# Optimization experiments

Hardware: AMD Instinct MI355X
Metric: run time of the kernel (lower is better)

Reference implementation:

```python
import jax, jax.numpy as jnp
import numpy as np

SLIDING_WINDOW = 2048
NUM_SINK = 4


def make_mask(q_len, k_len, dtype=jnp.float32):
    # positions of queries in the key axis
    q_pos = jnp.arange(k_len - q_len, k_len)[:, None]  # [Q,1]
    k_pos = jnp.arange(k_len)[None, :]                 # [1,K]
    causal = k_pos <= q_pos
    in_window = k_pos >= (q_pos - SLIDING_WINDOW + 1)
    is_sink = k_pos < NUM_SINK
    allowed = causal & (in_window | is_sink)
    return jnp.where(allowed, jnp.zeros((), dtype), jnp.full((), -jnp.inf, dtype))


def setup_inputs() -> dict:
    key = jax.random.key(0)
    k1, k2, k3 = jax.random.split(key, 3)
    B, H, L, D = 2, 16, 4096, 128
    q = jax.random.normal(k1, (B, H, L, D), dtype=jnp.float32)
    k = jax.random.normal(k2, (B, H, L, D), dtype=jnp.float32)
    v = jax.random.normal(k3, (B, H, L, D), dtype=jnp.float32)
    return {"q": q, "k": k, "v": v}


def reference(q, k, v):
    B, H, L, D = q.shape
    mask = make_mask(L, k.shape[2], q.dtype)  # [L, L] additive
    scale = 1.0 / jnp.sqrt(jnp.asarray(D, q.dtype))
    scores = jnp.einsum('bhqd,bhkd->bhqk', q, k) * scale + mask
    probs = jax.nn.softmax(scores, axis=-1)
    return jnp.einsum('bhqk,bhkd->bhqd', probs, v)
```

## Files before the change

kernel.cpp:

```cpp
#include <hip/hip_runtime.h>

constexpr int Ld = 4096;
constexpr int Dd = 128;
constexpr int BQ = 128;
constexpr int BK = 64;
constexpr int WSZ = 2048;
constexpr int NSINK = 4;
constexpr float QSCALE = 0.08838834764831845f * 1.4426950408889634f;

typedef short bf16x8 __attribute__((ext_vector_type(8)));
typedef float f32x4 __attribute__((ext_vector_type(4)));

#if defined(__has_builtin)
#if __has_builtin(__builtin_amdgcn_exp2f)
#define EXP2(x) __builtin_amdgcn_exp2f(x)
#endif
#endif
#ifndef EXP2
#define EXP2(x) exp2f(x)
#endif

__device__ __forceinline__ unsigned pkbf(float hi, float lo) {
    unsigned r;
    asm("v_cvt_pk_bf16_f32 %0, %1, %2" : "=v"(r) : "v"(lo), "v"(hi));
    return r;
}

__device__ __forceinline__ int rd_off(int row, int d) {
    return row * 128 + ((((d >> 3) ^ row) & 15) << 3) + (d & 7);
}
__device__ __forceinline__ int vt_off(int drow, int key) {
    return drow * 64 + ((((key >> 3) ^ drow) & 7) << 3) + (key & 7);
}
__device__ __forceinline__ int p_off(int row, int key) {
    return row * 64 + ((((key >> 2) ^ ((row & 7) << 1)) & 15) << 2) + (key & 3);
}

__global__ __launch_bounds__(256, 2)
void swa_fwd(const float* __restrict__ Qg, const float* __restrict__ Kg,
             const float* __restrict__ Vg, float* __restrict__ Og) {
    __shared__ __align__(16) unsigned short smem[24576];
    unsigned short* Ks  = smem;
    unsigned short* Vts = smem + 8192;
    unsigned short* Ps  = smem + 16384;
    unsigned short* Qst = smem;

    const int tid  = threadIdx.x;
    const int w    = tid >> 6;
    const int lane = tid & 63;
    const int ml   = lane & 15;
    const int quad = lane >> 4;

    const int qtile = (int)(gridDim.x - 1u - blockIdx.x);
    const int q0 = qtile * BQ;
    const int bh = blockIdx.y;

    const size_t baseQ  = ((size_t)bh * Ld + q0) * Dd;
    const size_t baseKV = (size_t)bh * Ld * Dd;

    #pragma unroll
    for (int i = 0; i < 16; ++i) {
        int idx = tid + i * 256;
        int row = idx >> 5;
        int d0  = (idx & 31) << 2;
        float4 v = *(const float4*)(Qg + baseQ + (size_t)row * Dd + d0);
        *(uint2*)&Qst[rd_off(row, d0)] =
            make_uint2(pkbf(v.y * QSCALE, v.x * QSCALE),
                       pkbf(v.w * QSCALE, v.z * QSCALE));
    }
    __syncthreads();

    bf16x8 qf[2][4];
    #pragma unroll
    for (int g = 0; g < 2; ++g)
        #pragma unroll
        for (int k0 = 0; k0 < 4; ++k0)
            qf[g][k0] = *(const bf16x8*)&Qst[rd_off(w * 32 + g * 16 + ml,
                                                    k0 * 32 + quad * 8)];

    float l_i[2] = {0.f, 0.f};
    f32x4 o_acc[2][8];
    #pragma unroll
    for (int g = 0; g < 2; ++g)
        #pragma unroll
        for (int dt = 0; dt < 8; ++dt)
            o_acc[g][dt] = (f32x4){0.f, 0.f, 0.f, 0.f};

    const int kmin = (q0 - (WSZ - 1)) > 0 ? (q0 - (WSZ - 1)) : 0;
    const int kb_first = (kmin / BK) * BK;
    const bool sink_extra = (kb_first > 0);
    const int nch = (q0 + BQ - kb_first) / BK + (sink_extra ? 1 : 0);

    const int qrow0 = q0 + w * 32 + ml;
    unsigned short* Pw = Ps + w * 2048;

    float4 kreg[8];
    float  vreg[32];
    const int kr0 = tid >> 5;
    const int kd0 = (tid & 31) << 2;
    const int vd  = tid & 127;
    const int vkh = tid >> 7;

    auto kvload = [&](int kb) {
        const float* kp = Kg + baseKV + (size_t)(kb + kr0) * Dd + kd0;
        #pragma unroll
        for (int i = 0; i < 8; ++i)
            kreg[i] = *(const float4*)(kp + (size_t)i * 8 * Dd);
        const float* vp = Vg + baseKV + (size_t)(kb + vkh * 32) * Dd + vd;
        #pragma unroll
        for (int j = 0; j < 32; ++j)
            vreg[j] = vp[(size_t)j * Dd];
    };
    auto kb_of = [&](int ci) {
        return sink_extra ? (ci == 0 ? 0 : kb_first + (ci - 1) * BK)
                          : kb_first + ci * BK;
    };

    kvload(kb_of(0));

    for (int ci = 0; ci < nch; ++ci) {
        const int kb = kb_of(ci);

        __syncthreads();

        #pragma unroll
        for (int i = 0; i < 8; ++i)
            *(uint2*)&Ks[rd_off(kr0 + i * 8, kd0)] =
                make_uint2(pkbf(kreg[i].y, kreg[i].x),
                           pkbf(kreg[i].w, kreg[i].z));
        #pragma unroll
        for (int m2 = 0; m2 < 4; ++m2) {
            *(uint4*)&Vts[vt_off(vd, vkh * 32 + m2 * 8)] =
                make_uint4(pkbf(vreg[m2 * 8 + 1], vreg[m2 * 8 + 0]),
                           pkbf(vreg[m2 * 8 + 3], vreg[m2 * 8 + 2]),
                           pkbf(vreg[m2 * 8 + 5], vreg[m2 * 8 + 4]),
                           pkbf(vreg[m2 * 8 + 7], vreg[m2 * 8 + 6]));
        }
        __syncthreads();

        if (ci + 1 < nch) kvload(kb_of(ci + 1));

        f32x4 s[2][4];
        #pragma unroll
        for (int g = 0; g < 2; ++g)
            #pragma unroll
            for (int t = 0; t < 4; ++t)
                s[g][t] = (f32x4){0.f, 0.f, 0.f, 0.f};
        #pragma unroll
        for (int k0 = 0; k0 < 4; ++k0) {
            bf16x8 ka[4];
            #pragma unroll
            for (int t = 0; t < 4; ++t)
                ka[t] = *(const bf16x8*)&Ks[rd_off(t * 16 + ml, k0 * 32 + quad * 8)];
            #pragma unroll
            for (int t = 0; t < 4; ++t) {
                s[0][t] = __builtin_amdgcn_mfma_f32_16x16x32_bf16(ka[t], qf[0][k0], s[0][t], 0, 0, 0);
                s[1][t] = __builtin_amdgcn_mfma_f32_16x16x32_bf16(ka[t], qf[1][k0], s[1][t], 0, 0, 0);
            }
        }

        const bool full = (kb + (BK - 1) <= q0) && (kb + (WSZ - BQ) >= q0 - 1);

        #pragma unroll
        for (int g = 0; g < 2; ++g) {
            const int q = qrow0 + g * 16;
            if (!full) {
                #pragma unroll
                for (int t = 0; t < 4; ++t)
                    #pragma unroll
                    for (int r = 0; r < 4; ++r) {
                        int k = kb + t * 16 + quad * 4 + r;
                        bool ok = (k <= q) && ((k + (WSZ - 1) >= q) || (k < NSINK));
                        s[g][t][r] = ok ? s[g][t][r] : -3e38f;
                    }
            }
            float rs = 0.f;
            #pragma unroll
            for (int t = 0; t < 4; ++t)
                #pragma unroll
                for (int r = 0; r < 4; ++r) {
                    float p = EXP2(s[g][t][r]);
                    s[g][t][r] = p;
                    rs += p;
                }
            l_i[g] += rs;

            unsigned short* Pg = Pw + g * 1024;
            #pragma unroll
            for (int t = 0; t < 4; ++t)
                *(uint2*)&Pg[p_off(ml, t * 16 + quad * 4)] =
                    make_uint2(pkbf(s[g][t][1], s[g][t][0]),
                               pkbf(s[g][t][3], s[g][t][2]));
        }

        #pragma unroll
        for (int k0 = 0; k0 < 2; ++k0) {
            bf16x8 pb0 = *(const bf16x8*)&Pw[p_off(ml, k0 * 32 + quad * 8)];
            bf16x8 pb1 = *(const bf16x8*)&Pw[1024 + p_off(ml, k0 * 32 + quad * 8)];
            #pragma unroll
            for (int dt = 0; dt < 8; ++dt) {
                bf16x8 va = *(const bf16x8*)&Vts[vt_off(dt * 16 + ml, k0 * 32 + quad * 8)];
                o_acc[0][dt] = __builtin_amdgcn_mfma_f32_16x16x32_bf16(va, pb0, o_acc[0][dt], 0, 0, 0);
                o_acc[1][dt] = __builtin_amdgcn_mfma_f32_16x16x32_bf16(va, pb1, o_acc[1][dt], 0, 0, 0);
            }
        }
    }

    #pragma unroll
    for (int g = 0; g < 2; ++g) {
        float lt = l_i[g];
        lt += __shfl_xor(lt, 16);
        lt += __shfl_xor(lt, 32);
        const float inv = 1.f / lt;
        float* op = Og + ((size_t)bh * Ld + (qrow0 + g * 16)) * Dd;
        #pragma unroll
        for (int dt = 0; dt < 8; ++dt) {
            float4 o;
            o.x = o_acc[g][dt][0] * inv;
            o.y = o_acc[g][dt][1] * inv;
            o.z = o_acc[g][dt][2] * inv;
            o.w = o_acc[g][dt][3] * inv;
            *(float4*)(op + dt * 16 + quad * 4) = o;
        }
    }
}

extern "C" void kernel_launch(void* const* d_in, const int* in_sizes, int n_in,
                              void* d_out, int out_size, void* d_ws, size_t ws_size,
                              hipStream_t stream) {
    const float* q = (const float*)d_in[0];
    const float* k = (const float*)d_in[1];
    const float* v = (const float*)d_in[2];
    float* o = (float*)d_out;
    const int bhn = in_sizes[0] / (Ld * Dd);
    dim3 grid(Ld / BQ, bhn);
    swa_fwd<<<grid, dim3(256, 1, 1), 0, stream>>>(q, k, v, o);
}
```

Measured before the change: 400.6 us.

## Pre-convert K/V to swizzled bf16 and stream tiles via async global-to-LDS loads

Adds a pre-pass kernel that converts K and V to bf16 once, with K in the swizzled row layout and V pre-transposed per 64-key block, and writes both into the workspace. The attention kernel then double-buffers K/V tiles in LDS using global_load_lds direct copies, which removes the per-tile fp32 register staging, repeated conversion, and one barrier per iteration. It also remaps workgroups with an XCD-aware 1D grid and raises wave priority around the MFMA sections. The trade-offs are an extra launch plus a bf16 write and read of K/V, and a larger LDS footprint (80 KB) that may limit occupancy to the two blocks the launch bounds target.

New measurement: 340.0 us. -15.1%, faster.

```diff
diff --git a/kernel.cpp b/kernel.cpp
--- a/kernel.cpp
+++ b/kernel.cpp
@@ -36,13 +36,58 @@
     return row * 64 + ((((key >> 2) ^ ((row & 7) << 1)) & 15) << 2) + (key & 3);
 }
 
+typedef const __attribute__((address_space(1))) unsigned int* gas1_t;
+typedef __attribute__((address_space(3))) unsigned int* las3_t;
+__device__ __forceinline__ void lds16(const void* g, void* l) {
+    __builtin_amdgcn_global_load_lds((gas1_t)g, (las3_t)l, 16, 0, 0);
+}
+
+__global__ __launch_bounds__(256)
+void cvt_kv(const float* __restrict__ Kg, const float* __restrict__ Vg,
+            unsigned short* __restrict__ Kw, unsigned short* __restrict__ Vw) {
+    __shared__ __align__(16) unsigned short vt[8192];
+    const int tid = threadIdx.x;
+    const int kb = blockIdx.x * BK;
+    const int bh = blockIdx.y;
+    const size_t gbase = ((size_t)bh * Ld + kb) * Dd;
+
+    #pragma unroll
+    for (int i = 0; i < 8; ++i) {
+        int id = tid + i * 256;
+        int row = id >> 5;
+        int d0 = (id & 31) << 2;
+        float4 a = *(const float4*)(Kg + gbase + (size_t)row * Dd + d0);
+        *(uint2*)&Kw[gbase + rd_off(row, d0)] =
+            make_uint2(pkbf(a.y, a.x), pkbf(a.w, a.z));
+    }
+
+    const int vd  = tid & 127;
+    const int vkh = tid >> 7;
+    const float* vp = Vg + gbase + (size_t)vkh * 32 * Dd + vd;
+    float vr[32];
+    #pragma unroll
+    for (int j = 0; j < 32; ++j) vr[j] = vp[(size_t)j * Dd];
+    #pragma unroll
+    for (int m2 = 0; m2 < 4; ++m2)
+        *(uint4*)&vt[vt_off(vd, vkh * 32 + m2 * 8)] =
+            make_uint4(pkbf(vr[m2 * 8 + 1], vr[m2 * 8 + 0]),
+                       pkbf(vr[m2 * 8 + 3], vr[m2 * 8 + 2]),
+                       pkbf(vr[m2 * 8 + 5], vr[m2 * 8 + 4]),
+                       pkbf(vr[m2 * 8 + 7], vr[m2 * 8 + 6]));
+    __syncthreads();
+    const size_t vbase = ((size_t)bh * (Ld / BK) + blockIdx.x) * (size_t)(BK * Dd);
+    #pragma unroll
+    for (int i = 0; i < 4; ++i) {
+        int j = tid + i * 256;
+        *(uint4*)&Vw[vbase + (size_t)j * 8] = *(const uint4*)&vt[j * 8];
+    }
+}
+
 __global__ __launch_bounds__(256, 2)
-void swa_fwd(const float* __restrict__ Qg, const float* __restrict__ Kg,
-             const float* __restrict__ Vg, float* __restrict__ Og) {
-    __shared__ __align__(16) unsigned short smem[24576];
-    unsigned short* Ks  = smem;
-    unsigned short* Vts = smem + 8192;
-    unsigned short* Ps  = smem + 16384;
+void swa_fwd2(const float* __restrict__ Qg, const unsigned short* __restrict__ Kw,
+              const unsigned short* __restrict__ Vw, float* __restrict__ Og) {
+    __shared__ __align__(16) unsigned short smem[40960];
+    unsigned short* Ps  = smem + 32768;
     unsigned short* Qst = smem;
 
     const int tid  = threadIdx.x;
@@ -51,12 +96,16 @@
     const int ml   = lane & 15;
     const int quad = lane >> 4;
 
-    const int qtile = (int)(gridDim.x - 1u - blockIdx.x);
+    const unsigned wgr = blockIdx.x;
+    const unsigned nwg = gridDim.x;
+    unsigned wgid = wgr;
+    if ((nwg & 7u) == 0u) wgid = (wgr & 7u) * (nwg >> 3) + (wgr >> 3);
+    const int tpb   = Ld / BQ;
+    const int bh    = (int)(wgid / (unsigned)tpb);
+    const int qtile = tpb - 1 - (int)(wgid % (unsigned)tpb);
     const int q0 = qtile * BQ;
-    const int bh = blockIdx.y;
-
-    const size_t baseQ  = ((size_t)bh * Ld + q0) * Dd;
-    const size_t baseKV = (size_t)bh * Ld * Dd;
+
+    const size_t baseQ = ((size_t)bh * Ld + q0) * Dd;
 
     #pragma unroll
     for (int i = 0; i < 16; ++i) {
@@ -77,6 +126,7 @@
         for (int k0 = 0; k0 < 4; ++k0)
             qf[g][k0] = *(const bf16x8*)&Qst[rd_off(w * 32 + g * 16 + ml,
                                                     k0 * 32 + quad * 8)];
+    __syncthreads();
 
     float l_i[2] = {0.f, 0.f};
     f32x4 o_acc[2][8];
@@ -94,51 +144,35 @@
     const int qrow0 = q0 + w * 32 + ml;
     unsigned short* Pw = Ps + w * 2048;
 
-    float4 kreg[8];
-    float  vreg[32];
-    const int kr0 = tid >> 5;
-    const int kd0 = (tid & 31) << 2;
-    const int vd  = tid & 127;
-    const int vkh = tid >> 7;
-
-    auto kvload = [&](int kb) {
-        const float* kp = Kg + baseKV + (size_t)(kb + kr0) * Dd + kd0;
-        #pragma unroll
-        for (int i = 0; i < 8; ++i)
-            kreg[i] = *(const float4*)(kp + (size_t)i * 8 * Dd);
-        const float* vp = Vg + baseKV + (size_t)(kb + vkh * 32) * Dd + vd;
-        #pragma unroll
-        for (int j = 0; j < 32; ++j)
-            vreg[j] = vp[(size_t)j * Dd];
-    };
     auto kb_of = [&](int ci) {
         return sink_extra ? (ci == 0 ? 0 : kb_first + (ci - 1) * BK)
                           : kb_first + ci * BK;
     };
-
-    kvload(kb_of(0));
+    const size_t kwbase = (size_t)bh * Ld * Dd;
+    const size_t vwbase = (size_t)bh * (Ld / BK) * (size_t)(BK * Dd);
+
+    auto stage = [&](int ci) {
+        const int b = ci & 1;
+        const int kb = kb_of(ci);
+        const unsigned short* kg = Kw + kwbase + (size_t)kb * Dd + tid * 8;
+        unsigned short* kl = smem + b * 8192 + tid * 8;
+        const unsigned short* vg = Vw + vwbase + (size_t)(kb >> 6) * (BK * Dd) + tid * 8;
+        unsigned short* vl = smem + 16384 + b * 8192 + tid * 8;
+        #pragma unroll
+        for (int i = 0; i < 4; ++i) lds16(kg + i * 2048, kl + i * 2048);
+        #pragma unroll
+        for (int i = 0; i < 4; ++i) lds16(vg + i * 2048, vl + i * 2048);
+    };
+
+    stage(0);
 
     for (int ci = 0; ci < nch; ++ci) {
+        __syncthreads();
+        if (ci + 1 < nch) stage(ci + 1);
+
         const int kb = kb_of(ci);
-
-        __syncthreads();
-
-        #pragma unroll
-        for (int i = 0; i < 8; ++i)
-            *(uint2*)&Ks[rd_off(kr0 + i * 8, kd0)] =
-                make_uint2(pkbf(kreg[i].y, kreg[i].x),
-                           pkbf(kreg[i].w, kreg[i].z));
-        #pragma unroll
-        for (int m2 = 0; m2 < 4; ++m2) {
-            *(uint4*)&Vts[vt_off(vd, vkh * 32 + m2 * 8)] =
-                make_uint4(pkbf(vreg[m2 * 8 + 1], vreg[m2 * 8 + 0]),
-                           pkbf(vreg[m2 * 8 + 3], vreg[m2 * 8 + 2]),
-                           pkbf(vreg[m2 * 8 + 5], vreg[m2 * 8 + 4]),
-                           pkbf(vreg[m2 * 8 + 7], vreg[m2 * 8 + 6]));
-        }
-        __syncthreads();
-
-        if (ci + 1 < nch) kvload(kb_of(ci + 1));
+        const unsigned short* Ksb = smem + (ci & 1) * 8192;
+        const unsigned short* Vtb = smem + 16384 + (ci & 1) * 8192;
 
         f32x4 s[2][4];
         #pragma unroll
@@ -146,18 +180,20 @@
             #pragma unroll
             for (int t = 0; t < 4; ++t)
                 s[g][t] = (f32x4){0.f, 0.f, 0.f, 0.f};
+        __builtin_amdgcn_s_setprio(1);
         #pragma unroll
         for (int k0 = 0; k0 < 4; ++k0) {
             bf16x8 ka[4];
             #pragma unroll
             for (int t = 0; t < 4; ++t)
-                ka[t] = *(const bf16x8*)&Ks[rd_off(t * 16 + ml, k0 * 32 + quad * 8)];
+                ka[t] = *(const bf16x8*)&Ksb[rd_off(t * 16 + ml, k0 * 32 + quad * 8)];
             #pragma unroll
             for (int t = 0; t < 4; ++t) {
                 s[0][t] = __builtin_amdgcn_mfma_f32_16x16x32_bf16(ka[t], qf[0][k0], s[0][t], 0, 0, 0);
                 s[1][t] = __builtin_amdgcn_mfma_f32_16x16x32_bf16(ka[t], qf[1][k0], s[1][t], 0, 0, 0);
             }
         }
+        __builtin_amdgcn_s_setprio(0);
 
         const bool full = (kb + (BK - 1) <= q0) && (kb + (WSZ - BQ) >= q0 - 1);
 
@@ -193,6 +229,194 @@
                                pkbf(s[g][t][3], s[g][t][2]));
         }
 
+        __builtin_amdgcn_s_setprio(1);
+        #pragma unroll
+        for (int k0 = 0; k0 < 2; ++k0) {
+            bf16x8 pb0 = *(const bf16x8*)&Pw[p_off(ml, k0 * 32 + quad * 8)];
+            bf16x8 pb1 = *(const bf16x8*)&Pw[1024 + p_off(ml, k0 * 32 + quad * 8)];
+            #pragma unroll
+            for (int dt = 0; dt < 8; ++dt) {
+                bf16x8 va = *(const bf16x8*)&Vtb[vt_off(dt * 16 + ml, k0 * 32 + quad * 8)];
+                o_acc[0][dt] = __builtin_amdgcn_mfma_f32_16x16x32_bf16(va, pb0, o_acc[0][dt], 0, 0, 0);
+                o_acc[1][dt] = __builtin_amdgcn_mfma_f32_16x16x32_bf16(va, pb1, o_acc[1][dt], 0, 0, 0);
+            }
+        }
+        __builtin_amdgcn_s_setprio(0);
+    }
+
+    #pragma unroll
+    for (int g = 0; g < 2; ++g) {
+        float lt = l_i[g];
+        lt += __shfl_xor(lt, 16);
+        lt += __shfl_xor(lt, 32);
+        const float inv = 1.f / lt;
+        float* op = Og + ((size_t)bh * Ld + (qrow0 + g * 16)) * Dd;
+        #pragma unroll
+        for (int dt = 0; dt < 8; ++dt) {
+            float4 o;
+            o.x = o_acc[g][dt][0] * inv;
+            o.y = o_acc[g][dt][1] * inv;
+            o.z = o_acc[g][dt][2] * inv;
+            o.w = o_acc[g][dt][3] * inv;
+            *(float4*)(op + dt * 16 + quad * 4) = o;
+        }
+    }
+}
+
+__global__ __launch_bounds__(256, 2)
+void swa_fwd(const float* __restrict__ Qg, const float* __restrict__ Kg,
+             const float* __restrict__ Vg, float* __restrict__ Og) {
+    __shared__ __align__(16) unsigned short smem[24576];
+    unsigned short* Ks  = smem;
+    unsigned short* Vts = smem + 8192;
+    unsigned short* Ps  = smem + 16384;
+    unsigned short* Qst = smem;
+
+    const int tid  = threadIdx.x;
+    const int w    = tid >> 6;
+    const int lane = tid & 63;
+    const int ml   = lane & 15;
+    const int quad = lane >> 4;
+
+    const int qtile = (int)(gridDim.x - 1u - blockIdx.x);
+    const int q0 = qtile * BQ;
+    const int bh = blockIdx.y;
+
+    const size_t baseQ  = ((size_t)bh * Ld + q0) * Dd;
+    const size_t baseKV = (size_t)bh * Ld * Dd;
+
+    #pragma unroll
+    for (int i = 0; i < 16; ++i) {
+        int idx = tid + i * 256;
+        int row = idx >> 5;
+        int d0  = (idx & 31) << 2;
+        float4 v = *(const float4*)(Qg + baseQ + (size_t)row * Dd + d0);
+        *(uint2*)&Qst[rd_off(row, d0)] =
+            make_uint2(pkbf(v.y * QSCALE, v.x * QSCALE),
+                       pkbf(v.w * QSCALE, v.z * QSCALE));
+    }
+    __syncthreads();
+
+    bf16x8 qf[2][4];
+    #pragma unroll
+    for (int g = 0; g < 2; ++g)
+        #pragma unroll
+        for (int k0 = 0; k0 < 4; ++k0)
+            qf[g][k0] = *(const bf16x8*)&Qst[rd_off(w * 32 + g * 16 + ml,
+                                                    k0 * 32 + quad * 8)];
+
+    float l_i[2] = {0.f, 0.f};
+    f32x4 o_acc[2][8];
+    #pragma unroll
+    for (int g = 0; g < 2; ++g)
+        #pragma unroll
+        for (int dt = 0; dt < 8; ++dt)
+            o_acc[g][dt] = (f32x4){0.f, 0.f, 0.f, 0.f};
+
+    const int kmin = (q0 - (WSZ - 1)) > 0 ? (q0 - (WSZ - 1)) : 0;
+    const int kb_first = (kmin / BK) * BK;
+    const bool sink_extra = (kb_first > 0);
+    const int nch = (q0 + BQ - kb_first) / BK + (sink_extra ? 1 : 0);
+
+    const int qrow0 = q0 + w * 32 + ml;
+    unsigned short* Pw = Ps + w * 2048;
+
+    float4 kreg[8];
+    float  vreg[32];
+    const int kr0 = tid >> 5;
+    const int kd0 = (tid & 31) << 2;
+    const int vd  = tid & 127;
+    const int vkh = tid >> 7;
+
+    auto kvload = [&](int kb) {
+        const float* kp = Kg + baseKV + (size_t)(kb + kr0) * Dd + kd0;
+        #pragma unroll
+        for (int i = 0; i < 8; ++i)
+            kreg[i] = *(const float4*)(kp + (size_t)i * 8 * Dd);
+        const float* vp = Vg + baseKV + (size_t)(kb + vkh * 32) * Dd + vd;
+        #pragma unroll
+        for (int j = 0; j < 32; ++j)
+            vreg[j] = vp[(size_t)j * Dd];
+    };
+    auto kb_of = [&](int ci) {
+        return sink_extra ? (ci == 0 ? 0 : kb_first + (ci - 1) * BK)
+                          : kb_first + ci * BK;
+    };
+
+    kvload(kb_of(0));
+
+    for (int ci = 0; ci < nch; ++ci) {
+        const int kb = kb_of(ci);
+        __syncthreads();
+        #pragma unroll
+        for (int i = 0; i < 8; ++i)
+            *(uint2*)&Ks[rd_off(kr0 + i * 8, kd0)] =
+                make_uint2(pkbf(kreg[i].y, kreg[i].x),
+                           pkbf(kreg[i].w, kreg[i].z));
+        #pragma unroll
+        for (int m2 = 0; m2 < 4; ++m2) {
+            *(uint4*)&Vts[vt_off(vd, vkh * 32 + m2 * 8)] =
+                make_uint4(pkbf(vreg[m2 * 8 + 1], vreg[m2 * 8 + 0]),
+                           pkbf(vreg[m2 * 8 + 3], vreg[m2 * 8 + 2]),
+                           pkbf(vreg[m2 * 8 + 5], vreg[m2 * 8 + 4]),
+                           pkbf(vreg[m2 * 8 + 7], vreg[m2 * 8 + 6]));
+        }
+        __syncthreads();
+        if (ci + 1 < nch) kvload(kb_of(ci + 1));
+
+        f32x4 s[2][4];
+        #pragma unroll
+        for (int g = 0; g < 2; ++g)
+            #pragma unroll
+            for (int t = 0; t < 4; ++t)
+                s[g][t] = (f32x4){0.f, 0.f, 0.f, 0.f};
+        #pragma unroll
+        for (int k0 = 0; k0 < 4; ++k0) {
+            bf16x8 ka[4];
+            #pragma unroll
+            for (int t = 0; t < 4; ++t)
+                ka[t] = *(const bf16x8*)&Ks[rd_off(t * 16 + ml, k0 * 32 + quad * 8)];
+            #pragma unroll
+            for (int t = 0; t < 4; ++t) {
+                s[0][t] = __builtin_amdgcn_mfma_f32_16x16x32_bf16(ka[t], qf[0][k0], s[0][t], 0, 0, 0);
+                s[1][t] = __builtin_amdgcn_mfma_f32_16x16x32_bf16(ka[t], qf[1][k0], s[1][t], 0, 0, 0);
+            }
+        }
+
+        const bool full = (kb + (BK - 1) <= q0) && (kb + (WSZ - BQ) >= q0 - 1);
+
+        #pragma unroll
+        for (int g = 0; g < 2; ++g) {
+            const int q = qrow0 + g * 16;
+            if (!full) {
+                #pragma unroll
+                for (int t = 0; t < 4; ++t)
+                    #pragma unroll
+                    for (int r = 0; r < 4; ++r) {
+                        int k = kb + t * 16 + quad * 4 + r;
+                        bool ok = (k <= q) && ((k + (WSZ - 1) >= q) || (k < NSINK));
+                        s[g][t][r] = ok ? s[g][t][r] : -3e38f;
+                    }
+            }
+            float rs = 0.f;
+            #pragma unroll
+            for (int t = 0; t < 4; ++t)
+                #pragma unroll
+                for (int r = 0; r < 4; ++r) {
+                    float p = EXP2(s[g][t][r]);
+                    s[g][t][r] = p;
+                    rs += p;
+                }
+            l_i[g] += rs;
+
+            unsigned short* Pg = Pw + g * 1024;
+            #pragma unroll
+            for (int t = 0; t < 4; ++t)
+                *(uint2*)&Pg[p_off(ml, t * 16 + quad * 4)] =
+                    make_uint2(pkbf(s[g][t][1], s[g][t][0]),
+                               pkbf(s[g][t][3], s[g][t][2]));
+        }
+
         #pragma unroll
         for (int k0 = 0; k0 < 2; ++k0) {
             bf16x8 pb0 = *(const bf16x8*)&Pw[p_off(ml, k0 * 32 + quad * 8)];
@@ -233,6 +457,15 @@
     const float* v = (const float*)d_in[2];
     float* o = (float*)d_out;
     const int bhn = in_sizes[0] / (Ld * Dd);
-    dim3 grid(Ld / BQ, bhn);
-    swa_fwd<<<grid, dim3(256, 1, 1), 0, stream>>>(q, k, v, o);
-}
+    const size_t elems = (size_t)bhn * Ld * Dd;
+    const size_t need = 2 * elems * sizeof(unsigned short);
+    if (d_ws != nullptr && ws_size >= need) {
+        unsigned short* Kw = (unsigned short*)d_ws;
+        unsigned short* Vw = Kw + elems;
+        cvt_kv<<<dim3(Ld / BK, bhn), dim3(256, 1, 1), 0, stream>>>(k, v, Kw, Vw);
+        swa_fwd2<<<dim3((unsigned)(bhn * (Ld / BQ))), dim3(256, 1, 1), 0, stream>>>(q, Kw, Vw, o);
+    } else {
+        dim3 grid(Ld / BQ, bhn);
+        swa_fwd<<<grid, dim3(256, 1, 1), 0, stream>>>(q, k, v, o);
+    }
+}
```
